# Performance work log

Hardware: AMD Instinct MI355X
Metric: run time of the kernel (lower is better)

## Reference

```python
import jax, jax.numpy as jnp
import numpy as np

B, D_IN, NQ, H = 65536, 385, 64, 16  # batch, input dim, num questions, head width
DIMS = [385, 512, 256, 192]


def setup_inputs() -> dict:
    key = jax.random.key(0)
    ks = jax.random.split(key, 12)
    s = 0.02
    inp = {
        "x": jax.random.normal(ks[0], (B, D_IN), jnp.float32),
        "W1": jax.random.normal(ks[1], (DIMS[0], DIMS[1]), jnp.float32) * s,
        "b1": jnp.zeros((DIMS[1],), jnp.float32),
        "W2": jax.random.normal(ks[2], (DIMS[1], DIMS[2]), jnp.float32) * s,
        "b2": jnp.zeros((DIMS[2],), jnp.float32),
        "W3": jax.random.normal(ks[3], (DIMS[2], DIMS[3]), jnp.float32) * s,
        "b3": jnp.zeros((DIMS[3],), jnp.float32),
        # all true/false heads stacked: layout [qid, correct, H] flattened on last axis
        "Wh": jax.random.normal(ks[4], (DIMS[3], NQ * 2 * H), jnp.float32) * s,
        "bh": jnp.zeros((NQ * 2 * H,), jnp.float32),
        "question_ids": jax.random.randint(ks[5], (B,), 0, NQ, jnp.int32),
        "is_correct": jax.random.randint(ks[6], (B,), 0, 2, jnp.int32),
    }
    return inp


def reference(x, W1, b1, W2, b2, W3, b3, Wh, bh, question_ids, is_correct):
    # shared trunk (dropout is identity at eval); activation = relu
    h = jax.nn.relu(x @ W1 + b1)          # [B, 512]
    h = jax.nn.relu(h @ W2 + b2)          # [B, 256]
    h = jax.nn.relu(h @ W3 + b3)          # [B, 192] shared features
    # compute all heads densely, then gather the per-row head slice —
    # equivalent to routing each row to its (question_id, is_correct) Linear head
    logits_all = h @ Wh + bh              # [B, NQ*2*H]
    base = (question_ids * 2 + is_correct) * H        # [B]
    idx = base[:, None] + jnp.arange(H)[None, :]      # [B, H]
    return jnp.take_along_axis(logits_all, idx, axis=1)  # [B, H]
```

## Files before the change

kernel.cpp:

```cpp
#include <hip/hip_runtime.h>
#include <hip/hip_bf16.h>

#define THREADS 1024
#define ROWS 128

typedef __attribute__((ext_vector_type(4))) float f32x4;
typedef __attribute__((ext_vector_type(8))) short s16x8;

__device__ __forceinline__ unsigned short bfbits(float f) {
  __bf16 h = (__bf16)f;
  return __builtin_bit_cast(unsigned short, h);
}
__device__ __forceinline__ float bf2f(unsigned short h) {
  unsigned u = ((unsigned)h) << 16;
  return __builtin_bit_cast(float, u);
}

__global__ void prep_kernel(const float* __restrict__ W1, const float* __restrict__ W2,
                            const float* __restrict__ W3, const float* __restrict__ Wh,
                            unsigned short* __restrict__ w1f, unsigned short* __restrict__ w2f,
                            unsigned short* __restrict__ w3f, unsigned short* __restrict__ whT) {
  int u = blockIdx.x * blockDim.x + threadIdx.x;
  const int U1 = 24576, U2 = 16384, U3 = 6144, U4 = 49152;
  if (u < U1) {
    int lane = u & 63, r = (u >> 6) & 31, c = u >> 11;
    int f  = r * 16 + (lane & 15);
    int kb = c * 32 + ((lane >> 4) << 3);
    s16x8 v;
    #pragma unroll
    for (int j = 0; j < 8; ++j) v[j] = (short)bfbits(W1[(kb + j) * 512 + f]);
    *(s16x8*)(w1f + (u << 3)) = v;
    return;
  }
  u -= U1;
  if (u < U2) {
    int lane = u & 63, r = (u >> 6) & 15, c = u >> 10;
    int f  = r * 16 + (lane & 15);
    int kb = c * 32 + ((lane >> 4) << 3);
    s16x8 v;
    #pragma unroll
    for (int j = 0; j < 8; ++j) v[j] = (short)bfbits(W2[(kb + j) * 256 + f]);
    *(s16x8*)(w2f + (u << 3)) = v;
    return;
  }
  u -= U2;
  if (u < U3) {
    int lane = u & 63, t = u >> 6;
    int c = t / 12, r = t - c * 12;
    int f  = r * 16 + (lane & 15);
    int kb = c * 32 + ((lane >> 4) << 3);
    s16x8 v;
    #pragma unroll
    for (int j = 0; j < 8; ++j) v[j] = (short)bfbits(W3[(kb + j) * 192 + f]);
    *(s16x8*)(w3f + (u << 3)) = v;
    return;
  }
  u -= U3;
  if (u < U4) {
    int j = u & 15, v2 = u >> 4;
    int fo = v2 % 24, head = v2 / 24;
    s16x8 v;
    #pragma unroll
    for (int i = 0; i < 8; ++i) v[i] = (short)bfbits(Wh[(fo * 8 + i) * 2048 + head * 16 + j]);
    *(s16x8*)(whT + u * 8) = v;
  }
}

#define MFMA(a, b, c) __builtin_amdgcn_mfma_f32_16x16x32_bf16((a), (b), (c), 0, 0, 0)
#define SWZ(lp) (((lp) * 16) ^ ((((lp) >> 4) & 3) << 5))

#define G1_RANGE(P, C0, C1)                                                          \
  _Pragma("unroll")                                                                  \
  for (int c = (C0); c < (C1); ++c) {                                                \
    s16x8 af = *(const s16x8*)(w1f + (((c * 32 + (P) * 16 + w) * 64 + lane) << 3));  \
    _Pragma("unroll")                                                                \
    for (int bt = 0; bt < 8; ++bt) {                                                 \
      s16x8 bfr = *(const s16x8*)(xall + (c << 13) + (bt << 10) + swz_l);            \
      acc1[bt] = MFMA(af, bfr, acc1[bt]);                                            \
    }                                                                                \
  }

__global__ __launch_bounds__(THREADS, 4)
void fused_mlp(const float* __restrict__ x,
               const float* __restrict__ b1,
               const float* __restrict__ b2,
               const float* __restrict__ b3,
               const float* __restrict__ bh,
               const float* __restrict__ W1,
               const int* __restrict__ qid,
               const int* __restrict__ corr,
               const unsigned short* __restrict__ w1f,
               const unsigned short* __restrict__ w2f,
               const unsigned short* __restrict__ w3f,
               const unsigned short* __restrict__ whT,
               float* __restrict__ out) {
  __shared__ __align__(16) unsigned char lds[163840];
  unsigned char*  xall = lds;
  unsigned char*  hL   = lds;
  unsigned short* h3b  = (unsigned short*)lds;
  unsigned char*  hH   = lds + 98304;
  unsigned char*  h2f  = lds + 98304;

  const int tid  = threadIdx.x;
  const int lane = tid & 63;
  const int w    = tid >> 6;
  const int b0   = blockIdx.x * ROWS;
  const int l15  = lane & 15;
  const int lh   = lane >> 4;
  const int swz_l = SWZ(lane);

  const int hrow = tid >> 4, hj = tid & 15;
  const int head0 = qid[b0 + hrow] * 2 + corr[b0 + hrow];
  const int head1 = qid[b0 + 64 + hrow] * 2 + corr[b0 + 64 + hrow];
  float xv384[8];
  #pragma unroll
  for (int bt = 0; bt < 8; ++bt)
    xv384[bt] = x[(size_t)(b0 + bt * 16 + l15) * 385 + 384];

  f32x4 sv[2][2];
  int s_ad[2];
  auto sload = [&](int g) {
    #pragma unroll
    for (int q = 0; q < 2; ++q) {
      int fi = q * 1024 + tid;
      int c  = (g << 2) + (fi >> 9);
      int wi = fi & 511;
      int bt = wi >> 6, lp = wi & 63;
      int row = (bt << 4) + (lp & 15);
      int k   = c * 32 + ((lp >> 4) << 3);
      const float* p = x + (size_t)(b0 + row) * 385 + k;
      sv[q][0] = *(const f32x4*)p;
      sv[q][1] = *(const f32x4*)(p + 4);
      s_ad[q] = (c << 13) + (bt << 10) + SWZ(lp);
    }
  };
  auto swrite = [&]() {
    #pragma unroll
    for (int q = 0; q < 2; ++q) {
      s16x8 v;
      v[0] = (short)bfbits(sv[q][0][0]); v[1] = (short)bfbits(sv[q][0][1]);
      v[2] = (short)bfbits(sv[q][0][2]); v[3] = (short)bfbits(sv[q][0][3]);
      v[4] = (short)bfbits(sv[q][1][0]); v[5] = (short)bfbits(sv[q][1][1]);
      v[6] = (short)bfbits(sv[q][1][2]); v[7] = (short)bfbits(sv[q][1][3]);
      *(s16x8*)(xall + s_ad[q]) = v;
    }
  };

  f32x4 acc1[8];
  #pragma unroll
  for (int bt = 0; bt < 8; ++bt) acc1[bt] = (f32x4)0.0f;

  auto epi1 = [&](int P, unsigned char* dst) {
    int fg = P * 256 + w * 16 + lh * 4;
    f32x4 bv = *(const f32x4*)(b1 + fg);
    f32x4 wv = *(const f32x4*)(W1 + 384 * 512 + fg);
    int so = ((w >> 1) << 13) + SWZ(l15 + (((2 * w + (lh >> 1)) & 3) << 4)) + ((lh & 1) << 3);
    #pragma unroll
    for (int bt = 0; bt < 8; ++bt) {
      float xv = xv384[bt];
      float v0 = fmaxf(acc1[bt][0] + bv[0] + wv[0] * xv, 0.f);
      float v1 = fmaxf(acc1[bt][1] + bv[1] + wv[1] * xv, 0.f);
      float v2 = fmaxf(acc1[bt][2] + bv[2] + wv[2] * xv, 0.f);
      float v3 = fmaxf(acc1[bt][3] + bv[3] + wv[3] * xv, 0.f);
      unsigned plo = (unsigned)bfbits(v0) | ((unsigned)bfbits(v1) << 16);
      unsigned phi = (unsigned)bfbits(v2) | ((unsigned)bfbits(v3) << 16);
      unsigned long long pk = (unsigned long long)plo | ((unsigned long long)phi << 32);
      *(unsigned long long*)(dst + so + (bt << 10)) = pk;
      acc1[bt] = (f32x4)0.0f;
    }
  };

  sload(0); swrite();
  __syncthreads();

  sload(1);
  G1_RANGE(0, 0, 4)
  swrite();
  __syncthreads();

  sload(2);
  G1_RANGE(0, 4, 8)
  swrite();
  __syncthreads();

  G1_RANGE(0, 8, 12)
  epi1(0, hH);

  G1_RANGE(1, 0, 12)
  __syncthreads();
  epi1(1, hL);
  __syncthreads();

  f32x4 acc2[8];
  #pragma unroll
  for (int bt = 0; bt < 8; ++bt) acc2[bt] = (f32x4)0.0f;

  #pragma unroll
  for (int c = 0; c < 8; ++c) {
    s16x8 a2 = *(const s16x8*)(w2f + (((c * 16 + w) * 64 + lane) << 3));
    #pragma unroll
    for (int bt = 0; bt < 8; ++bt) {
      s16x8 bfr = *(const s16x8*)(hH + (c << 13) + (bt << 10) + swz_l);
      acc2[bt] = MFMA(a2, bfr, acc2[bt]);
    }
  }
  #pragma unroll
  for (int c = 8; c < 16; ++c) {
    s16x8 a2 = *(const s16x8*)(w2f + (((c * 16 + w) * 64 + lane) << 3));
    #pragma unroll
    for (int bt = 0; bt < 8; ++bt) {
      s16x8 bfr = *(const s16x8*)(hL + ((c - 8) << 13) + (bt << 10) + swz_l);
      acc2[bt] = MFMA(a2, bfr, acc2[bt]);
    }
  }
  __syncthreads();

  {
    int fg = w * 16 + lh * 4;
    f32x4 bv = *(const f32x4*)(b2 + fg);
    int so = ((w >> 1) << 13) + SWZ(l15 + (((2 * w + (lh >> 1)) & 3) << 4)) + ((lh & 1) << 3);
    #pragma unroll
    for (int bt = 0; bt < 8; ++bt) {
      float v0 = fmaxf(acc2[bt][0] + bv[0], 0.f);
      float v1 = fmaxf(acc2[bt][1] + bv[1], 0.f);
      float v2 = fmaxf(acc2[bt][2] + bv[2], 0.f);
      float v3 = fmaxf(acc2[bt][3] + bv[3], 0.f);
      unsigned plo = (unsigned)bfbits(v0) | ((unsigned)bfbits(v1) << 16);
      unsigned phi = (unsigned)bfbits(v2) | ((unsigned)bfbits(v3) << 16);
      unsigned long long pk = (unsigned long long)plo | ((unsigned long long)phi << 32);
      *(unsigned long long*)(h2f + so + (bt << 10)) = pk;
    }
  }
  __syncthreads();

  if (w < 12) {
    f32x4 acc3[8];
    #pragma unroll
    for (int bt = 0; bt < 8; ++bt) acc3[bt] = (f32x4)0.0f;
    #pragma unroll
    for (int c = 0; c < 8; ++c) {
      s16x8 a3 = *(const s16x8*)(w3f + (((c * 12 + w) * 64 + lane) << 3));
      #pragma unroll
      for (int bt = 0; bt < 8; ++bt) {
        s16x8 bfr = *(const s16x8*)(h2f + (c << 13) + (bt << 10) + swz_l);
        acc3[bt] = MFMA(a3, bfr, acc3[bt]);
      }
    }
    int fg = w * 16 + lh * 4;
    f32x4 bv = *(const f32x4*)(b3 + fg);
    #pragma unroll
    for (int bt = 0; bt < 8; ++bt) {
      int row = (bt << 4) + l15;
      float v0 = fmaxf(acc3[bt][0] + bv[0], 0.f);
      float v1 = fmaxf(acc3[bt][1] + bv[1], 0.f);
      float v2 = fmaxf(acc3[bt][2] + bv[2], 0.f);
      float v3 = fmaxf(acc3[bt][3] + bv[3], 0.f);
      unsigned plo = (unsigned)bfbits(v0) | ((unsigned)bfbits(v1) << 16);
      unsigned phi = (unsigned)bfbits(v2) | ((unsigned)bfbits(v3) << 16);
      unsigned long long pk = (unsigned long long)plo | ((unsigned long long)phi << 32);
      *(unsigned long long*)((unsigned char*)h3b + row * 400 + w * 32 + lh * 8) = pk;
    }
  }
  __syncthreads();

  #pragma unroll
  for (int q = 0; q < 2; ++q) {
    int row  = q * 64 + hrow;
    int head = q ? head1 : head0;
    const unsigned short* wp = whT + ((head * 24) * 16 + hj) * 8;
    const unsigned short* hp = h3b + row * 200;
    float acc = bh[(head << 4) + hj];
    #pragma unroll 6
    for (int fo = 0; fo < 24; ++fo) {
      s16x8 wv = *(const s16x8*)(wp + fo * 128);
      s16x8 hv = *(const s16x8*)(hp + fo * 8);
      #pragma unroll
      for (int e = 0; e < 8; ++e)
        acc += bf2f((unsigned short)wv[e]) * bf2f((unsigned short)hv[e]);
    }
    out[(size_t)(b0 + row) * 16 + hj] = acc;
  }
}

extern "C" void kernel_launch(void* const* d_in, const int* in_sizes, int n_in,
                              void* d_out, int out_size, void* d_ws, size_t ws_size,
                              hipStream_t stream) {
  (void)in_sizes; (void)n_in; (void)out_size; (void)ws_size;
  const float* x  = (const float*)d_in[0];
  const float* W1 = (const float*)d_in[1];
  const float* b1 = (const float*)d_in[2];
  const float* W2 = (const float*)d_in[3];
  const float* b2 = (const float*)d_in[4];
  const float* W3 = (const float*)d_in[5];
  const float* b3 = (const float*)d_in[6];
  const float* Wh = (const float*)d_in[7];
  const float* bh = (const float*)d_in[8];
  const int* qid  = (const int*)d_in[9];
  const int* corr = (const int*)d_in[10];
  float* out = (float*)d_out;

  unsigned short* w1f = (unsigned short*)d_ws;
  unsigned short* w2f = w1f + 12 * 32 * 64 * 8;
  unsigned short* w3f = w2f + 16 * 16 * 64 * 8;
  unsigned short* whT = w3f + 8 * 12 * 64 * 8;

  prep_kernel<<<376, 256, 0, stream>>>(W1, W2, W3, Wh, w1f, w2f, w3f, whT);
  fused_mlp<<<65536 / ROWS, THREADS, 0, stream>>>(x, b1, b2, b3, bh, W1, qid, corr,
                                                  w1f, w2f, w3f, whT, out);
}
```

Measured before the change: 106.1 us.

## Pipeline x staging in finer chunks and defer per-row loads to cut registers

The x tile is now staged in six groups of two k-chunks instead of three groups of four. Each thread holds one 8-float staging slot instead of two, and load addresses are precomputed once. The x[:,384] column and the head indices are loaded where they are used rather than kept live from kernel start. This lowers register pressure in the layer-1 loop, in exchange for more block-wide barriers and shorter windows for overlapping global loads with MFMA work.

```diff
diff --git a/kernel.cpp b/kernel.cpp
--- a/kernel.cpp
+++ b/kernel.cpp
@@ -109,41 +109,27 @@
   const int lh   = lane >> 4;
   const int swz_l = SWZ(lane);
 
-  const int hrow = tid >> 4, hj = tid & 15;
-  const int head0 = qid[b0 + hrow] * 2 + corr[b0 + hrow];
-  const int head1 = qid[b0 + 64 + hrow] * 2 + corr[b0 + 64 + hrow];
-  float xv384[8];
-  #pragma unroll
-  for (int bt = 0; bt < 8; ++bt)
-    xv384[bt] = x[(size_t)(b0 + bt * 16 + l15) * 385 + 384];
-
-  f32x4 sv[2][2];
-  int s_ad[2];
+  const int s_wi  = tid & 511;
+  const int s_ci  = tid >> 9;
+  const int s_bt  = s_wi >> 6;
+  const int s_lp  = s_wi & 63;
+  const float* s_base = x + (size_t)(b0 + (s_bt << 4) + (s_lp & 15)) * 385 + ((s_lp >> 4) << 3);
+  const int s_abase = (s_bt << 10) + SWZ(s_lp);
+
+  f32x4 sv0, sv1;
   auto sload = [&](int g) {
-    #pragma unroll
-    for (int q = 0; q < 2; ++q) {
-      int fi = q * 1024 + tid;
-      int c  = (g << 2) + (fi >> 9);
-      int wi = fi & 511;
-      int bt = wi >> 6, lp = wi & 63;
-      int row = (bt << 4) + (lp & 15);
-      int k   = c * 32 + ((lp >> 4) << 3);
-      const float* p = x + (size_t)(b0 + row) * 385 + k;
-      sv[q][0] = *(const f32x4*)p;
-      sv[q][1] = *(const f32x4*)(p + 4);
-      s_ad[q] = (c << 13) + (bt << 10) + SWZ(lp);
-    }
+    int c = (g << 1) + s_ci;
+    sv0 = *(const f32x4*)(s_base + c * 32);
+    sv1 = *(const f32x4*)(s_base + c * 32 + 4);
   };
-  auto swrite = [&]() {
-    #pragma unroll
-    for (int q = 0; q < 2; ++q) {
-      s16x8 v;
-      v[0] = (short)bfbits(sv[q][0][0]); v[1] = (short)bfbits(sv[q][0][1]);
-      v[2] = (short)bfbits(sv[q][0][2]); v[3] = (short)bfbits(sv[q][0][3]);
-      v[4] = (short)bfbits(sv[q][1][0]); v[5] = (short)bfbits(sv[q][1][1]);
-      v[6] = (short)bfbits(sv[q][1][2]); v[7] = (short)bfbits(sv[q][1][3]);
-      *(s16x8*)(xall + s_ad[q]) = v;
-    }
+  auto swrite = [&](int g) {
+    int c = (g << 1) + s_ci;
+    s16x8 v;
+    v[0] = (short)bfbits(sv0[0]); v[1] = (short)bfbits(sv0[1]);
+    v[2] = (short)bfbits(sv0[2]); v[3] = (short)bfbits(sv0[3]);
+    v[4] = (short)bfbits(sv1[0]); v[5] = (short)bfbits(sv1[1]);
+    v[6] = (short)bfbits(sv1[2]); v[7] = (short)bfbits(sv1[3]);
+    *(s16x8*)(xall + (c << 13) + s_abase) = v;
   };
 
   f32x4 acc1[8];
@@ -157,7 +143,7 @@
     int so = ((w >> 1) << 13) + SWZ(l15 + (((2 * w + (lh >> 1)) & 3) << 4)) + ((lh & 1) << 3);
     #pragma unroll
     for (int bt = 0; bt < 8; ++bt) {
-      float xv = xv384[bt];
+      float xv = x[(size_t)(b0 + (bt << 4) + l15) * 385 + 384];
       float v0 = fmaxf(acc1[bt][0] + bv[0] + wv[0] * xv, 0.f);
       float v1 = fmaxf(acc1[bt][1] + bv[1] + wv[1] * xv, 0.f);
       float v2 = fmaxf(acc1[bt][2] + bv[2] + wv[2] * xv, 0.f);
@@ -170,20 +156,16 @@
     }
   };
 
-  sload(0); swrite();
-  __syncthreads();
-
-  sload(1);
-  G1_RANGE(0, 0, 4)
-  swrite();
-  __syncthreads();
-
-  sload(2);
-  G1_RANGE(0, 4, 8)
-  swrite();
-  __syncthreads();
-
-  G1_RANGE(0, 8, 12)
+  sload(0); swrite(0);
+  __syncthreads();
+
+  sload(1); G1_RANGE(0, 0, 2)  swrite(1); __syncthreads();
+  sload(2); G1_RANGE(0, 2, 4)  swrite(2); __syncthreads();
+  sload(3); G1_RANGE(0, 4, 6)  swrite(3); __syncthreads();
+  sload(4); G1_RANGE(0, 6, 8)  swrite(4); __syncthreads();
+  sload(5); G1_RANGE(0, 8, 10) swrite(5); __syncthreads();
+
+  G1_RANGE(0, 10, 12)
   epi1(0, hH);
 
   G1_RANGE(1, 0, 12)
@@ -232,6 +214,10 @@
     }
   }
   __syncthreads();
+
+  const int hrow = tid >> 4, hj = tid & 15;
+  const int head0 = qid[b0 + hrow] * 2 + corr[b0 + hrow];
+  const int head1 = qid[b0 + 64 + hrow] * 2 + corr[b0 + 64 + hrow];
 
   if (w < 12) {
     f32x4 acc3[8];
```

Measured after the change: 103.4 us. 1.03x faster.
